# Optimization experiments

Measured on AMD Instinct MI355X. Metric: run time of the kernel, lower is better.

Reference implementation:

```python
import jax, jax.numpy as jnp
import numpy as np

BN_EPS = 1e-5


def conv1d(x, w, stride, pad):
    # x: [N, C, T], w: [O, I, K]
    return jax.lax.conv_general_dilated(
        x, w, window_strides=(stride,), padding=[(pad, pad)],
        dimension_numbers=('NCH', 'OIH', 'NCH'))


def setup_inputs() -> dict:
    key = jax.random.key(0)
    ks = jax.random.split(key, 10)
    B, Cin, T = 32, 80, 1024
    C, D, M = 768, 64, 512
    s = 0.02
    inp = {
        'mels': jax.random.normal(ks[0], (B, Cin, T), jnp.float32),
        'w1': jax.random.normal(ks[1], (C, Cin, 3), jnp.float32) * s,
        'w2': jax.random.normal(ks[2], (C, C, 3), jnp.float32) * s,
        'w3': jax.random.normal(ks[3], (C, C, 4), jnp.float32) * s,
        'w4': jax.random.normal(ks[4], (C, C, 3), jnp.float32) * s,
        'w5': jax.random.normal(ks[5], (C, C, 3), jnp.float32) * s,
        'w6': jax.random.normal(ks[6], (D, C, 1), jnp.float32) * s,
        'b6': jnp.zeros((D,), jnp.float32),
        'bn_gamma': jnp.ones((5, C), jnp.float32),
        'bn_beta': jnp.zeros((5, C), jnp.float32),
        'bn_mean': jnp.zeros((5, C), jnp.float32),
        'bn_var': jnp.ones((5, C), jnp.float32),
        'embedding': jax.random.uniform(ks[7], (M, D), jnp.float32,
                                        minval=-1.0 / 512, maxval=1.0 / 512),
    }
    return inp


def reference(mels, w1, w2, w3, w4, w5, w6, b6,
              bn_gamma, bn_beta, bn_mean, bn_var, embedding):
    def block(x, w, stride, pad, i):
        x = conv1d(x, w, stride, pad)
        inv = bn_gamma[i] / jnp.sqrt(bn_var[i] + BN_EPS)
        x = x * inv[None, :, None] + (bn_beta[i] - bn_mean[i] * inv)[None, :, None]
        return jax.nn.relu(x)

    z = block(mels, w1, 1, 0, 0)   # [B, C, 1022]
    z = block(z, w2, 1, 1, 1)
    z = block(z, w3, 2, 1, 2)      # [B, C, 511]
    z = block(z, w4, 1, 1, 3)
    z = block(z, w5, 1, 1, 4)
    z = conv1d(z, w6, 1, 0) + b6[None, :, None]  # [B, D, 511]
    z = jnp.transpose(z, (0, 2, 1))              # [B, T', D]

    B, Tp, D = z.shape
    M = embedding.shape[0]
    x_flat = jax.lax.stop_gradient(z).reshape(-1, D)  # [N, D]
    dists = (jnp.sum(embedding ** 2, axis=1)[None, :]
             + jnp.sum(x_flat ** 2, axis=1, keepdims=True)
             - 2.0 * x_flat @ embedding.T)
    idx = jnp.argmin(dists, axis=-1)                  # [N]
    quantized = embedding[idx].reshape(B, Tp, D)
    loss = 0.25 * jnp.mean((z - jax.lax.stop_gradient(quantized)) ** 2)
    q_st = z + jax.lax.stop_gradient(quantized - z)   # straight-through
    counts = jnp.zeros((M,), jnp.float32).at[idx].add(1.0)
    avg_probs = counts / idx.shape[0]
    perplexity = jnp.exp(-jnp.sum(avg_probs * jnp.log(avg_probs + 1e-10)))
    return (q_st, loss, perplexity)
```

## Files before the change

kernel.cpp:

```cpp
#include <hip/hip_runtime.h>
#include <cstddef>
#include <cstdint>

#define BN_EPS 1e-5f

typedef _Float16 half8 __attribute__((ext_vector_type(8)));
typedef float f32x4v __attribute__((ext_vector_type(4)));

__device__ __forceinline__ unsigned split_pack(float v) {
    _Float16 h = (_Float16)v;
    float r = (v - (float)h) * 2048.0f;
    _Float16 l = (_Float16)r;
    unsigned short hu = __builtin_bit_cast(unsigned short, h);
    unsigned short lu = __builtin_bit_cast(unsigned short, l);
    return (unsigned)hu | ((unsigned)lu << 16);
}

__global__ __launch_bounds__(256)
void prep_w(const float* __restrict__ w, unsigned* __restrict__ wp,
            int Cin, int KW, int CIPAD)
{
    int id = blockIdx.x * 256 + threadIdx.x;
    int total = KW * 768 * CIPAD;
    if (id >= total) return;
    int cip = id % CIPAD;
    int co  = (id / CIPAD) % 768;
    int kw  = id / (CIPAD * 768);
    float v = 0.0f;
    if (cip < Cin) v = w[((size_t)co * Cin + cip) * KW + kw];
    wp[id] = split_pack(v * 256.0f);
}

__global__ __launch_bounds__(256)
void prep_mels(const float* __restrict__ mels, unsigned* __restrict__ mt)
{
    int id = blockIdx.x * 256 + threadIdx.x;
    if (id >= 32 * 1032 * 96) return;
    int c = id % 96;
    int t = (id / 96) % 1032;
    int b = id / (96 * 1032);
    float v = 0.0f;
    if (c < 80 && t < 1024) v = mels[((size_t)b * 80 + c) * 1024 + t];
    mt[id] = split_pack(v * 16.0f);
}

template<int KW, int S, int P, int CIPAD, int TIN, int TSIN, int TOUT, int TSOUT, int EPI>
__global__ __launch_bounds__(256)
void conv_mfma(const unsigned* __restrict__ Xin, const unsigned* __restrict__ Wp,
               const float* __restrict__ gamma, const float* __restrict__ beta,
               const float* __restrict__ mean, const float* __restrict__ var,
               unsigned* __restrict__ Uout, float* __restrict__ Fout)
{
    constexpr int NCI = CIPAD / 32;
    constexpr int NC  = KW * NCI;
    __shared__ unsigned smem[16896];
    _Float16* sm = (_Float16*)smem;

    const int b   = blockIdx.z;
    const int co0 = blockIdx.x * 128;
    const int t0  = blockIdx.y * 128;
    const int tid = threadIdx.x;
    const int lane = tid & 63, wv = tid >> 6;
    const int quad = lane >> 4, l16 = lane & 15;
    const int wm = (wv & 1) * 64, wn = (wv >> 1) * 64;

    f32x4v accH[4][4] = {};
    f32x4v accX[4][4] = {};

    const int srow = tid >> 1;
    const int sh   = tid & 1;
    const unsigned* __restrict__ xb = Xin + (size_t)b * TSIN * CIPAD;

    uint4 rA[4], rB[4];

    auto loadAB = [&](int c) {
        const int kw  = c / NCI;
        const int ci0 = (c % NCI) * 32;
        const unsigned* pA = Wp + (size_t)(kw * 768 + co0 + srow) * CIPAD + ci0;
        rA[0] = *(const uint4*)(pA + sh * 8);
        rA[1] = *(const uint4*)(pA + sh * 8 + 4);
        rA[2] = *(const uint4*)(pA + (sh + 2) * 8);
        rA[3] = *(const uint4*)(pA + (sh + 2) * 8 + 4);
        const int tp = (t0 + srow) * S + kw - P;
        rB[0] = rB[1] = rB[2] = rB[3] = make_uint4(0, 0, 0, 0);
        if ((unsigned)tp < (unsigned)TIN) {
            const unsigned* pB = xb + (size_t)tp * CIPAD + ci0;
            rB[0] = *(const uint4*)(pB + sh * 8);
            rB[1] = *(const uint4*)(pB + sh * 8 + 4);
            rB[2] = *(const uint4*)(pB + (sh + 2) * 8);
            rB[3] = *(const uint4*)(pB + (sh + 2) * 8 + 4);
        }
    };

    auto splitHL = [](uint4 a, uint4 b2, uint4& h, uint4& l) {
        h.x = (a.x & 0xffffu) | (a.y << 16);
        h.y = (a.z & 0xffffu) | (a.w << 16);
        h.z = (b2.x & 0xffffu) | (b2.y << 16);
        h.w = (b2.z & 0xffffu) | (b2.w << 16);
        l.x = (a.x >> 16) | (a.y & 0xffff0000u);
        l.y = (a.z >> 16) | (a.w & 0xffff0000u);
        l.z = (b2.x >> 16) | (b2.y & 0xffff0000u);
        l.w = (b2.z >> 16) | (b2.w & 0xffff0000u);
    };

    auto storeAB = [&](int pbuf) {
        const int b0 = pbuf * 16384;
        const int u1 = (((srow >> 4) * 4 + sh) * 16 + (srow & 15)) * 8;
        const int u2 = u1 + 256;
        uint4 h, l;
        splitHL(rA[0], rA[1], h, l);
        *(uint4*)(sm + b0 + 0     + u1) = h;
        *(uint4*)(sm + b0 + 4096  + u1) = l;
        splitHL(rA[2], rA[3], h, l);
        *(uint4*)(sm + b0 + 0     + u2) = h;
        *(uint4*)(sm + b0 + 4096  + u2) = l;
        splitHL(rB[0], rB[1], h, l);
        *(uint4*)(sm + b0 + 8192  + u1) = h;
        *(uint4*)(sm + b0 + 12288 + u1) = l;
        splitHL(rB[2], rB[3], h, l);
        *(uint4*)(sm + b0 + 8192  + u2) = h;
        *(uint4*)(sm + b0 + 12288 + u2) = l;
    };

    loadAB(0);
    storeAB(0);
    if (NC > 1) loadAB(1);
    __syncthreads();

    int p = 0;
    for (int c = 0; c < NC; ++c) {
        const int base = p * 16384;
        if (c + 1 < NC) storeAB(p ^ 1);
        if (c + 2 < NC) loadAB(c + 2);

        half8 bh[4], bl[4];
#pragma unroll
        for (int nt = 0; nt < 4; ++nt) {
            int gn = (wv >> 1) * 4 + nt;
            int u = ((gn * 4 + quad) * 16 + l16) * 8;
            bh[nt] = *(const half8*)(sm + base + 8192  + u);
            bl[nt] = *(const half8*)(sm + base + 12288 + u);
        }
#pragma unroll
        for (int mt = 0; mt < 4; ++mt) {
            int gm = (wv & 1) * 4 + mt;
            int u = ((gm * 4 + quad) * 16 + l16) * 8;
            half8 ah = *(const half8*)(sm + base + 0    + u);
            half8 al = *(const half8*)(sm + base + 4096 + u);
#pragma unroll
            for (int nt = 0; nt < 4; ++nt) {
                accH[mt][nt] = __builtin_amdgcn_mfma_f32_16x16x32_f16(ah, bh[nt], accH[mt][nt], 0, 0, 0);
                accX[mt][nt] = __builtin_amdgcn_mfma_f32_16x16x32_f16(ah, bl[nt], accX[mt][nt], 0, 0, 0);
                accX[mt][nt] = __builtin_amdgcn_mfma_f32_16x16x32_f16(al, bh[nt], accX[mt][nt], 0, 0, 0);
            }
        }
        __syncthreads();
        p ^= 1;
    }

    if constexpr (EPI == 0) {
        unsigned* bb = smem;
#pragma unroll
        for (int mt = 0; mt < 4; ++mt) {
#pragma unroll
            for (int r = 0; r < 4; ++r) {
                int mloc = wm + mt * 16 + quad * 4 + r;
                int co = co0 + mloc;
                float iv = gamma[co] / sqrtf(var[co] + BN_EPS);
                float sh2 = beta[co] - mean[co] * iv;
#pragma unroll
                for (int nt = 0; nt < 4; ++nt) {
                    float vf = (accH[mt][nt][r] + accX[mt][nt][r] * (1.0f / 2048.0f)) * (1.0f / 4096.0f);
                    float y = fmaf(vf, iv, sh2);
                    y = y > 0.0f ? y : 0.0f;
                    bb[(wn + nt * 16 + l16) * 132 + mloc] = split_pack(y * 16.0f);
                }
            }
        }
        __syncthreads();
        int tl = tid >> 1, seg = tid & 1;
        int t = t0 + tl;
        if (t < TOUT) {
            uint4* dst = (uint4*)(Uout + ((size_t)b * TSOUT + t) * 768 + co0 + seg * 64);
            const uint4* src = (const uint4*)(bb + tl * 132 + seg * 64);
#pragma unroll
            for (int i = 0; i < 16; ++i) dst[i] = src[i];
        }
    } else {
#pragma unroll
        for (int mt = 0; mt < 4; ++mt) {
#pragma unroll
            for (int r = 0; r < 4; ++r) {
                int co = co0 + wm + mt * 16 + quad * 4 + r;
                float iv = gamma[co] / sqrtf(var[co] + BN_EPS);
                float sh2 = beta[co] - mean[co] * iv;
                float* op = Fout + ((size_t)b * 768 + co) * TOUT;
#pragma unroll
                for (int nt = 0; nt < 4; ++nt) {
                    int t = t0 + wn + nt * 16 + l16;
                    if (t < TOUT) {
                        float vf = (accH[mt][nt][r] + accX[mt][nt][r] * (1.0f / 2048.0f)) * (1.0f / 4096.0f);
                        float y = fmaf(vf, iv, sh2);
                        op[t] = y > 0.0f ? y : 0.0f;
                    }
                }
            }
        }
    }
}

constexpr int TM = 64, TN = 64, TK = 16;

__global__ __launch_bounds__(256)
void conv1x1_bias_T(const float* __restrict__ in, const float* __restrict__ w,
                    const float* __restrict__ bias, float* __restrict__ z,
                    int Cin, int T)
{
    const int b   = blockIdx.z;
    const int t0  = blockIdx.y * TN;
    const int tid = threadIdx.x;

    __shared__ float As[TK][TM + 4];
    __shared__ float Bs[TK][TN + 4];

    float acc[4][4] = {};

    const int m0 = (tid & 15) * 4;
    const int n0 = (tid >> 4) * 4;

    const float* __restrict__ inb = in + (size_t)b * Cin * T;

    const int a_m = tid >> 4;
    const int a_k = tid & 15;
    const int b_k = tid >> 6;
    const int b_n = tid & 63;

    for (int kc = 0; kc < Cin; kc += TK) {
        __syncthreads();
#pragma unroll
        for (int i = 0; i < 4; ++i) {
            int m = a_m + 16 * i;
            As[a_k][m] = w[(size_t)m * Cin + kc + a_k];
        }
#pragma unroll
        for (int i = 0; i < 4; ++i) {
            int kk = b_k + 4 * i;
            int ci = kc + kk;
            int t  = t0 + b_n;
            Bs[kk][b_n] = (t < T) ? inb[(size_t)ci * T + t] : 0.0f;
        }
        __syncthreads();
#pragma unroll
        for (int kk = 0; kk < TK; ++kk) {
            float4 av = *reinterpret_cast<const float4*>(&As[kk][m0]);
            float4 bv = *reinterpret_cast<const float4*>(&Bs[kk][n0]);
            float am[4] = {av.x, av.y, av.z, av.w};
            float bn[4] = {bv.x, bv.y, bv.z, bv.w};
#pragma unroll
            for (int mi = 0; mi < 4; ++mi)
#pragma unroll
                for (int nj = 0; nj < 4; ++nj)
                    acc[mi][nj] = fmaf(am[mi], bn[nj], acc[mi][nj]);
        }
    }

    float4 bb = *reinterpret_cast<const float4*>(&bias[m0]);
    float bs[4] = {bb.x, bb.y, bb.z, bb.w};
#pragma unroll
    for (int nj = 0; nj < 4; ++nj) {
        int t = t0 + n0 + nj;
        if (t < T) {
            float4 v;
            v.x = acc[0][nj] + bs[0];
            v.y = acc[1][nj] + bs[1];
            v.z = acc[2][nj] + bs[2];
            v.w = acc[3][nj] + bs[3];
            *reinterpret_cast<float4*>(&z[((size_t)b * T + t) * 64 + m0]) = v;
        }
    }
}

__global__ __launch_bounds__(256)
void vq_e2(const float* __restrict__ emb, float* __restrict__ e2)
{
    int m = blockIdx.x * 256 + threadIdx.x;
    if (m < 512) {
        float s = 0.0f;
#pragma unroll
        for (int d = 0; d < 64; ++d) {
            float v = emb[(size_t)m * 64 + d];
            s = fmaf(v, v, s);
        }
        e2[m] = s;
    }
}

__global__ __launch_bounds__(64)
void vq_argmin(const float* __restrict__ z, const float* __restrict__ emb,
               const float* __restrict__ e2, int* __restrict__ idx,
               float* __restrict__ counts, int N)
{
    __shared__ float Es[64 * 64];
    const int tid = threadIdx.x;
    const int n   = blockIdx.x * 64 + tid;
    const bool act = n < N;

    float x[64];
    float x2 = 0.0f;
    if (act) {
        const float4* zp = reinterpret_cast<const float4*>(z + (size_t)n * 64);
#pragma unroll
        for (int i = 0; i < 16; ++i) {
            float4 v = zp[i];
            x[4 * i + 0] = v.x; x[4 * i + 1] = v.y;
            x[4 * i + 2] = v.z; x[4 * i + 3] = v.w;
        }
#pragma unroll
        for (int d = 0; d < 64; ++d) x2 = fmaf(x[d], x[d], x2);
    }

    float best = 3.4e38f;
    int   bi   = 0;
    for (int c = 0; c < 8; ++c) {
        __syncthreads();
        const float4* ep  = reinterpret_cast<const float4*>(emb + (size_t)c * 4096);
        float4*       esp = reinterpret_cast<float4*>(Es);
#pragma unroll
        for (int i = 0; i < 16; ++i) esp[tid + 64 * i] = ep[tid + 64 * i];
        __syncthreads();
        for (int r = 0; r < 64; ++r) {
            const float4* er = reinterpret_cast<const float4*>(&Es[r * 64]);
            float dot = 0.0f;
#pragma unroll
            for (int i = 0; i < 16; ++i) {
                float4 e4 = er[i];
                dot = fmaf(x[4 * i + 0], e4.x, dot);
                dot = fmaf(x[4 * i + 1], e4.y, dot);
                dot = fmaf(x[4 * i + 2], e4.z, dot);
                dot = fmaf(x[4 * i + 3], e4.w, dot);
            }
            float dist = (e2[c * 64 + r] + x2) - 2.0f * dot;
            if (dist < best) { best = dist; bi = c * 64 + r; }
        }
    }
    if (act) {
        idx[n] = bi;
        atomicAdd(&counts[bi], 1.0f);
    }
}

__global__ __launch_bounds__(256)
void vq_quant_loss(const float* __restrict__ z, const float* __restrict__ emb,
                   const int* __restrict__ idx, float* __restrict__ qout,
                   double* __restrict__ loss_sum, int Ntot)
{
    int g = blockIdx.x * 256 + threadIdx.x;
    float d2 = 0.0f;
    if (g < Ntot) {
        int n = g >> 6;
        int d = g & 63;
        float q  = emb[(size_t)idx[n] * 64 + d];
        float zv = z[g];
        qout[g] = zv + (q - zv);
        float diff = zv - q;
        d2 = diff * diff;
    }
#pragma unroll
    for (int o = 32; o > 0; o >>= 1) d2 += __shfl_down(d2, o);
    __shared__ float wsum[4];
    if ((threadIdx.x & 63) == 0) wsum[threadIdx.x >> 6] = d2;
    __syncthreads();
    if (threadIdx.x == 0)
        atomicAdd(loss_sum, (double)(wsum[0] + wsum[1] + wsum[2] + wsum[3]));
}

__global__ __launch_bounds__(512)
void vq_finalize(const float* __restrict__ counts, const double* __restrict__ loss_sum,
                 float* __restrict__ out, int Ntot, int Npts)
{
    int t = threadIdx.x;
    float c   = counts[t];
    float avg = c / (float)Npts;
    float term = avg * logf(avg + 1e-10f);
#pragma unroll
    for (int o = 32; o > 0; o >>= 1) term += __shfl_down(term, o);
    __shared__ float wsum[8];
    if ((t & 63) == 0) wsum[t >> 6] = term;
    __syncthreads();
    if (t == 0) {
        float s = 0.0f;
        for (int i = 0; i < 8; ++i) s += wsum[i];
        out[Ntot]     = 0.25f * (float)(loss_sum[0] / (double)Ntot);
        out[Ntot + 1] = expf(-s);
    }
}

extern "C" void kernel_launch(void* const* d_in, const int* in_sizes, int n_in,
                              void* d_out, int out_size, void* d_ws, size_t ws_size,
                              hipStream_t stream)
{
    const float* mels     = (const float*)d_in[0];
    const float* w1       = (const float*)d_in[1];
    const float* w2       = (const float*)d_in[2];
    const float* w3       = (const float*)d_in[3];
    const float* w4       = (const float*)d_in[4];
    const float* w5       = (const float*)d_in[5];
    const float* w6       = (const float*)d_in[6];
    const float* b6       = (const float*)d_in[7];
    const float* bn_gamma = (const float*)d_in[8];
    const float* bn_beta  = (const float*)d_in[9];
    const float* bn_mean  = (const float*)d_in[10];
    const float* bn_var   = (const float*)d_in[11];
    const float* emb      = (const float*)d_in[12];

    constexpr int B = 32, C = 768, D = 64, T2 = 511;

    char* ws = (char*)d_ws;
    unsigned* P1 = (unsigned*)ws;
    unsigned* P2 = (unsigned*)(ws + 100663296);
    unsigned* Wp = (unsigned*)(ws + 201326592);
    size_t misc  = 201326592 + 9437184;
    float*  counts = (float*)(ws + misc);
    double* lossp  = (double*)(ws + misc + 2048);
    float*  e2p    = (float*)(ws + misc + 2048 + 64);
    int*    idx    = (int*)(ws + misc + 2048 + 64 + 2048);

    unsigned* melsT = P2;
    float*    bufA  = (float*)P1;
    float*    z     = (float*)P2;

    hipMemsetAsync(ws + misc, 0, 2048 + 64, stream);

    vq_e2<<<dim3(2), 256, 0, stream>>>(emb, e2p);
    prep_mels<<<dim3((32 * 1032 * 96 + 255) / 256), 256, 0, stream>>>(mels, melsT);

    prep_w<<<dim3((3 * 768 * 96 + 255) / 256), 256, 0, stream>>>(w1, Wp, 80, 3, 96);
    conv_mfma<3, 1, 0, 96, 1032, 1032, 1022, 1024, 0><<<dim3(6, 8, B), 256, 0, stream>>>(
        melsT, Wp, bn_gamma + 0 * C, bn_beta + 0 * C, bn_mean + 0 * C, bn_var + 0 * C, P1, nullptr);
    prep_w<<<dim3((3 * 768 * 768 + 255) / 256), 256, 0, stream>>>(w2, Wp, 768, 3, 768);
    conv_mfma<3, 1, 1, 768, 1022, 1024, 1022, 1024, 0><<<dim3(6, 8, B), 256, 0, stream>>>(
        P1, Wp, bn_gamma + 1 * C, bn_beta + 1 * C, bn_mean + 1 * C, bn_var + 1 * C, P2, nullptr);
    prep_w<<<dim3((4 * 768 * 768 + 255) / 256), 256, 0, stream>>>(w3, Wp, 768, 4, 768);
    conv_mfma<4, 2, 1, 768, 1022, 1024, 511, 512, 0><<<dim3(6, 4, B), 256, 0, stream>>>(
        P2, Wp, bn_gamma + 2 * C, bn_beta + 2 * C, bn_mean + 2 * C, bn_var + 2 * C, P1, nullptr);
    prep_w<<<dim3((3 * 768 * 768 + 255) / 256), 256, 0, stream>>>(w4, Wp, 768, 3, 768);
    conv_mfma<3, 1, 1, 768, 511, 512, 511, 512, 0><<<dim3(6, 4, B), 256, 0, stream>>>(
        P1, Wp, bn_gamma + 3 * C, bn_beta + 3 * C, bn_mean + 3 * C, bn_var + 3 * C, P2, nullptr);
    prep_w<<<dim3((3 * 768 * 768 + 255) / 256), 256, 0, stream>>>(w5, Wp, 768, 3, 768);
    conv_mfma<3, 1, 1, 768, 511, 512, 511, 511, 1><<<dim3(6, 4, B), 256, 0, stream>>>(
        P2, Wp, bn_gamma + 4 * C, bn_beta + 4 * C, bn_mean + 4 * C, bn_var + 4 * C, nullptr, bufA);

    conv1x1_bias_T<<<dim3(1, 8, B), 256, 0, stream>>>(bufA, w6, b6, z, C, T2);

    const int Npts = B * T2;
    const int Ntot = Npts * D;
    vq_argmin<<<dim3((Npts + 63) / 64), 64, 0, stream>>>(z, emb, e2p, idx, counts, Npts);
    vq_quant_loss<<<dim3(Ntot / 256), 256, 0, stream>>>(z, emb, idx, (float*)d_out, lossp, Ntot);
    vq_finalize<<<dim3(1), 512, 0, stream>>>(counts, lossp, (float*)d_out, Ntot, Npts);
}
```

Baseline: 1.719 ms.

## Pre-layout weights as MFMA fragments and load A directly from global

Weights are pre-split into separate fp16 hi/lo arrays laid out in MFMA fragment order, so each wave loads its A operands straight from global/L2 and no longer stages them in LDS. This halves the LDS footprint, which may raise occupancy, and removes the A split/store work. The epilogue now writes packed outputs directly to global instead of transposing through LDS. The trade-off is that A loads are no longer double-buffered and are issued inside the loop right before the MFMAs, so they can expose global latency, and the direct epilogue stores are less coalesced.

```diff
diff --git a/kernel.cpp b/kernel.cpp
--- a/kernel.cpp
+++ b/kernel.cpp
@@ -17,18 +17,30 @@
 }
 
 __global__ __launch_bounds__(256)
-void prep_w(const float* __restrict__ w, unsigned* __restrict__ wp,
-            int Cin, int KW, int CIPAD)
+void prep_w_frag(const float* __restrict__ w, _Float16* __restrict__ Wh,
+                 _Float16* __restrict__ Wl, int Cin, int KW, int NCI)
 {
     int id = blockIdx.x * 256 + threadIdx.x;
-    int total = KW * 768 * CIPAD;
+    int total = KW * NCI * 48 * 4 * 16;
     if (id >= total) return;
-    int cip = id % CIPAD;
-    int co  = (id / CIPAD) % 768;
-    int kw  = id / (CIPAD * 768);
-    float v = 0.0f;
-    if (cip < Cin) v = w[((size_t)co * Cin + cip) * KW + kw];
-    wp[id] = split_pack(v * 256.0f);
+    int m16  = id & 15;
+    int quad = (id >> 4) & 3;
+    int ct   = (id >> 6) % 48;
+    int c    = id / (48 * 4 * 16);
+    int kw   = c / NCI;
+    int cic  = c - kw * NCI;
+    int co   = ct * 16 + m16;
+    _Float16 h[8], l[8];
+#pragma unroll
+    for (int j = 0; j < 8; ++j) {
+        int ci = cic * 32 + quad * 8 + j;
+        float v = (ci < Cin) ? w[((size_t)co * Cin + ci) * KW + kw] * 256.0f : 0.0f;
+        _Float16 hh = (_Float16)v;
+        h[j] = hh;
+        l[j] = (_Float16)((v - (float)hh) * 2048.0f);
+    }
+    *(half8*)(Wh + (size_t)id * 8) = *(half8*)h;
+    *(half8*)(Wl + (size_t)id * 8) = *(half8*)l;
 }
 
 __global__ __launch_bounds__(256)
@@ -46,14 +58,15 @@
 
 template<int KW, int S, int P, int CIPAD, int TIN, int TSIN, int TOUT, int TSOUT, int EPI>
 __global__ __launch_bounds__(256)
-void conv_mfma(const unsigned* __restrict__ Xin, const unsigned* __restrict__ Wp,
+void conv_mfma(const unsigned* __restrict__ Xin,
+               const _Float16* __restrict__ Wh, const _Float16* __restrict__ Wl,
                const float* __restrict__ gamma, const float* __restrict__ beta,
                const float* __restrict__ mean, const float* __restrict__ var,
                unsigned* __restrict__ Uout, float* __restrict__ Fout)
 {
     constexpr int NCI = CIPAD / 32;
     constexpr int NC  = KW * NCI;
-    __shared__ unsigned smem[16896];
+    __shared__ unsigned smem[8192];
     _Float16* sm = (_Float16*)smem;
 
     const int b   = blockIdx.z;
@@ -63,6 +76,7 @@
     const int lane = tid & 63, wv = tid >> 6;
     const int quad = lane >> 4, l16 = lane & 15;
     const int wm = (wv & 1) * 64, wn = (wv >> 1) * 64;
+    const int ct0 = (co0 >> 4) + (wv & 1) * 4;
 
     f32x4v accH[4][4] = {};
     f32x4v accX[4][4] = {};
@@ -71,16 +85,11 @@
     const int sh   = tid & 1;
     const unsigned* __restrict__ xb = Xin + (size_t)b * TSIN * CIPAD;
 
-    uint4 rA[4], rB[4];
-
-    auto loadAB = [&](int c) {
+    uint4 rB[4];
+
+    auto loadB = [&](int c) {
         const int kw  = c / NCI;
         const int ci0 = (c % NCI) * 32;
-        const unsigned* pA = Wp + (size_t)(kw * 768 + co0 + srow) * CIPAD + ci0;
-        rA[0] = *(const uint4*)(pA + sh * 8);
-        rA[1] = *(const uint4*)(pA + sh * 8 + 4);
-        rA[2] = *(const uint4*)(pA + (sh + 2) * 8);
-        rA[3] = *(const uint4*)(pA + (sh + 2) * 8 + 4);
         const int tp = (t0 + srow) * S + kw - P;
         rB[0] = rB[1] = rB[2] = rB[3] = make_uint4(0, 0, 0, 0);
         if ((unsigned)tp < (unsigned)TIN) {
@@ -103,55 +112,55 @@
         l.w = (b2.z >> 16) | (b2.w & 0xffff0000u);
     };
 
-    auto storeAB = [&](int pbuf) {
-        const int b0 = pbuf * 16384;
+    auto storeB = [&](int pbuf) {
+        const int b0 = pbuf * 8192;
         const int u1 = (((srow >> 4) * 4 + sh) * 16 + (srow & 15)) * 8;
         const int u2 = u1 + 256;
         uint4 h, l;
-        splitHL(rA[0], rA[1], h, l);
-        *(uint4*)(sm + b0 + 0     + u1) = h;
-        *(uint4*)(sm + b0 + 4096  + u1) = l;
-        splitHL(rA[2], rA[3], h, l);
-        *(uint4*)(sm + b0 + 0     + u2) = h;
-        *(uint4*)(sm + b0 + 4096  + u2) = l;
         splitHL(rB[0], rB[1], h, l);
-        *(uint4*)(sm + b0 + 8192  + u1) = h;
-        *(uint4*)(sm + b0 + 12288 + u1) = l;
+        *(uint4*)(sm + b0 + 0    + u1) = h;
+        *(uint4*)(sm + b0 + 4096 + u1) = l;
         splitHL(rB[2], rB[3], h, l);
-        *(uint4*)(sm + b0 + 8192  + u2) = h;
-        *(uint4*)(sm + b0 + 12288 + u2) = l;
+        *(uint4*)(sm + b0 + 0    + u2) = h;
+        *(uint4*)(sm + b0 + 4096 + u2) = l;
     };
 
-    loadAB(0);
-    storeAB(0);
-    if (NC > 1) loadAB(1);
+    loadB(0);
+    storeB(0);
+    if (NC > 1) loadB(1);
     __syncthreads();
+
+    const int fo = (quad * 16 + l16) * 8;
 
     int p = 0;
     for (int c = 0; c < NC; ++c) {
-        const int base = p * 16384;
-        if (c + 1 < NC) storeAB(p ^ 1);
-        if (c + 2 < NC) loadAB(c + 2);
+        const int base = p * 8192;
+        if (c + 1 < NC) storeB(p ^ 1);
+        if (c + 2 < NC) loadB(c + 2);
+
+        half8 ah[4], al[4];
+#pragma unroll
+        for (int mt = 0; mt < 4; ++mt) {
+            size_t au = ((size_t)(c * 48 + ct0 + mt) * 512) + fo;
+            ah[mt] = *(const half8*)(Wh + au);
+            al[mt] = *(const half8*)(Wl + au);
+        }
 
         half8 bh[4], bl[4];
 #pragma unroll
         for (int nt = 0; nt < 4; ++nt) {
             int gn = (wv >> 1) * 4 + nt;
             int u = ((gn * 4 + quad) * 16 + l16) * 8;
-            bh[nt] = *(const half8*)(sm + base + 8192  + u);
-            bl[nt] = *(const half8*)(sm + base + 12288 + u);
+            bh[nt] = *(const half8*)(sm + base + u);
+            bl[nt] = *(const half8*)(sm + base + 4096 + u);
         }
 #pragma unroll
         for (int mt = 0; mt < 4; ++mt) {
-            int gm = (wv & 1) * 4 + mt;
-            int u = ((gm * 4 + quad) * 16 + l16) * 8;
-            half8 ah = *(const half8*)(sm + base + 0    + u);
-            half8 al = *(const half8*)(sm + base + 4096 + u);
 #pragma unroll
             for (int nt = 0; nt < 4; ++nt) {
-                accH[mt][nt] = __builtin_amdgcn_mfma_f32_16x16x32_f16(ah, bh[nt], accH[mt][nt], 0, 0, 0);
-                accX[mt][nt] = __builtin_amdgcn_mfma_f32_16x16x32_f16(ah, bl[nt], accX[mt][nt], 0, 0, 0);
-                accX[mt][nt] = __builtin_amdgcn_mfma_f32_16x16x32_f16(al, bh[nt], accX[mt][nt], 0, 0, 0);
+                accH[mt][nt] = __builtin_amdgcn_mfma_f32_16x16x32_f16(ah[mt], bh[nt], accH[mt][nt], 0, 0, 0);
+                accX[mt][nt] = __builtin_amdgcn_mfma_f32_16x16x32_f16(ah[mt], bl[nt], accX[mt][nt], 0, 0, 0);
+                accX[mt][nt] = __builtin_amdgcn_mfma_f32_16x16x32_f16(al[mt], bh[nt], accX[mt][nt], 0, 0, 0);
             }
         }
         __syncthreads();
@@ -159,32 +168,33 @@
     }
 
     if constexpr (EPI == 0) {
-        unsigned* bb = smem;
 #pragma unroll
         for (int mt = 0; mt < 4; ++mt) {
+            int cob = co0 + wm + mt * 16 + quad * 4;
+            float iv[4], sh2[4];
 #pragma unroll
             for (int r = 0; r < 4; ++r) {
-                int mloc = wm + mt * 16 + quad * 4 + r;
-                int co = co0 + mloc;
-                float iv = gamma[co] / sqrtf(var[co] + BN_EPS);
-                float sh2 = beta[co] - mean[co] * iv;
-#pragma unroll
-                for (int nt = 0; nt < 4; ++nt) {
-                    float vf = (accH[mt][nt][r] + accX[mt][nt][r] * (1.0f / 2048.0f)) * (1.0f / 4096.0f);
-                    float y = fmaf(vf, iv, sh2);
-                    y = y > 0.0f ? y : 0.0f;
-                    bb[(wn + nt * 16 + l16) * 132 + mloc] = split_pack(y * 16.0f);
+                int co = cob + r;
+                iv[r]  = gamma[co] / sqrtf(var[co] + BN_EPS);
+                sh2[r] = beta[co] - mean[co] * iv[r];
+            }
+#pragma unroll
+            for (int nt = 0; nt < 4; ++nt) {
+                int t = t0 + wn + nt * 16 + l16;
+                if (t < TOUT) {
+                    uint4 o;
+                    unsigned ov[4];
+#pragma unroll
+                    for (int r = 0; r < 4; ++r) {
+                        float vf = (accH[mt][nt][r] + accX[mt][nt][r] * (1.0f / 2048.0f)) * (1.0f / 4096.0f);
+                        float y = fmaf(vf, iv[r], sh2[r]);
+                        y = y > 0.0f ? y : 0.0f;
+                        ov[r] = split_pack(y * 16.0f);
+                    }
+                    o.x = ov[0]; o.y = ov[1]; o.z = ov[2]; o.w = ov[3];
+                    *(uint4*)(Uout + ((size_t)b * TSOUT + t) * 768 + cob) = o;
                 }
             }
-        }
-        __syncthreads();
-        int tl = tid >> 1, seg = tid & 1;
-        int t = t0 + tl;
-        if (t < TOUT) {
-            uint4* dst = (uint4*)(Uout + ((size_t)b * TSOUT + t) * 768 + co0 + seg * 64);
-            const uint4* src = (const uint4*)(bb + tl * 132 + seg * 64);
-#pragma unroll
-            for (int i = 0; i < 16; ++i) dst[i] = src[i];
         }
     } else {
 #pragma unroll
@@ -416,9 +426,10 @@
     constexpr int B = 32, C = 768, D = 64, T2 = 511;
 
     char* ws = (char*)d_ws;
-    unsigned* P1 = (unsigned*)ws;
-    unsigned* P2 = (unsigned*)(ws + 100663296);
-    unsigned* Wp = (unsigned*)(ws + 201326592);
+    unsigned*  P1 = (unsigned*)ws;
+    unsigned*  P2 = (unsigned*)(ws + 100663296);
+    _Float16*  Wh = (_Float16*)(ws + 201326592);
+    _Float16*  Wl = (_Float16*)(ws + 201326592 + 4718592);
     size_t misc  = 201326592 + 9437184;
     float*  counts = (float*)(ws + misc);
     double* lossp  = (double*)(ws + misc + 2048);
@@ -434,21 +445,21 @@
     vq_e2<<<dim3(2), 256, 0, stream>>>(emb, e2p);
     prep_mels<<<dim3((32 * 1032 * 96 + 255) / 256), 256, 0, stream>>>(mels, melsT);
 
-    prep_w<<<dim3((3 * 768 * 96 + 255) / 256), 256, 0, stream>>>(w1, Wp, 80, 3, 96);
+    prep_w_frag<<<dim3((3 * 3 * 3072 + 255) / 256), 256, 0, stream>>>(w1, Wh, Wl, 80, 3, 3);
     conv_mfma<3, 1, 0, 96, 1032, 1032, 1022, 1024, 0><<<dim3(6, 8, B), 256, 0, stream>>>(
-        melsT, Wp, bn_gamma + 0 * C, bn_beta + 0 * C, bn_mean + 0 * C, bn_var + 0 * C, P1, nullptr);
-    prep_w<<<dim3((3 * 768 * 768 + 255) / 256), 256, 0, stream>>>(w2, Wp, 768, 3, 768);
+        melsT, Wh, Wl, bn_gamma + 0 * C, bn_beta + 0 * C, bn_mean + 0 * C, bn_var + 0 * C, P1, nullptr);
+    prep_w_frag<<<dim3((3 * 24 * 3072 + 255) / 256), 256, 0, stream>>>(w2, Wh, Wl, 768, 3, 24);
     conv_mfma<3, 1, 1, 768, 1022, 1024, 1022, 1024, 0><<<dim3(6, 8, B), 256, 0, stream>>>(
-        P1, Wp, bn_gamma + 1 * C, bn_beta + 1 * C, bn_mean + 1 * C, bn_var + 1 * C, P2, nullptr);
-    prep_w<<<dim3((4 * 768 * 768 + 255) / 256), 256, 0, stream>>>(w3, Wp, 768, 4, 768);
+        P1, Wh, Wl, bn_gamma + 1 * C, bn_beta + 1 * C, bn_mean + 1 * C, bn_var + 1 * C, P2, nullptr);
+    prep_w_frag<<<dim3((4 * 24 * 3072 + 255) / 256), 256, 0, stream>>>(w3, Wh, Wl, 768, 4, 24);
     conv_mfma<4, 2, 1, 768, 1022, 1024, 511, 512, 0><<<dim3(6, 4, B), 256, 0, stream>>>(
-        P2, Wp, bn_gamma + 2 * C, bn_beta + 2 * C, bn_mean + 2 * C, bn_var + 2 * C, P1, nullptr);
-    prep_w<<<dim3((3 * 768 * 768 + 255) / 256), 256, 0, stream>>>(w4, Wp, 768, 3, 768);
+        P2, Wh, Wl, bn_gamma + 2 * C, bn_beta + 2 * C, bn_mean + 2 * C, bn_var + 2 * C, P1, nullptr);
+    prep_w_frag<<<dim3((3 * 24 * 3072 + 255) / 256), 256, 0, stream>>>(w4, Wh, Wl, 768, 3, 24);
     conv_mfma<3, 1, 1, 768, 511, 512, 511, 512, 0><<<dim3(6, 4, B), 256, 0, stream>>>(
-        P1, Wp, bn_gamma + 3 * C, bn_beta + 3 * C, bn_mean + 3 * C, bn_var + 3 * C, P2, nullptr);
-    prep_w<<<dim3((3 * 768 * 768 + 255) / 256), 256, 0, stream>>>(w5, Wp, 768, 3, 768);
+        P1, Wh, Wl, bn_gamma + 3 * C, bn_beta + 3 * C, bn_mean + 3 * C, bn_var + 3 * C, P2, nullptr);
+    prep_w_frag<<<dim3((3 * 24 * 3072 + 255) / 256), 256, 0, stream>>>(w5, Wh, Wl, 768, 3, 24);
     conv_mfma<3, 1, 1, 768, 511, 512, 511, 511, 1><<<dim3(6, 4, B), 256, 0, stream>>>(
-        P2, Wp, bn_gamma + 4 * C, bn_beta + 4 * C, bn_mean + 4 * C, bn_var + 4 * C, nullptr, bufA);
+        P2, Wh, Wl, bn_gamma + 4 * C, bn_beta + 4 * C, bn_mean + 4 * C, bn_var + 4 * C, nullptr, bufA);
 
     conv1x1_bias_T<<<dim3(1, 8, B), 256, 0, stream>>>(bufA, w6, b6, z, C, T2);
 
```

Result: slower. 2.148 ms (+24.9%).
